# Kernel optimization log

Measured on AMD Instinct MI355X. Metric: run time of the kernel, lower is better.

The kernel has to match this reference:

```python
import jax, jax.numpy as jnp
import numpy as np

B, T, HID = 4, 2048, 1024
H, DK, DV, K = 8, 64, 128, 4
EPS = 1e-5


def _dw_causal_conv(x, w, b):
    # x: (B,T,C), w: (C,1,K) depthwise, b: (C,). Causal: left-pad K-1.
    xt = jnp.transpose(x, (0, 2, 1))  # (B,C,T)
    y = jax.lax.conv_general_dilated(
        xt, w, window_strides=(1,), padding=[(K - 1, 0)],
        dimension_numbers=("NCH", "OIH", "NCH"), feature_group_count=x.shape[-1])
    y = y + b[None, :, None]
    return jnp.transpose(y, (0, 2, 1))  # (B,T,C)


def setup_inputs() -> dict:
    key = jax.random.key(0)
    ks = jax.random.split(key, 20)
    s = 0.02
    inp = {
        "x": jax.random.normal(ks[0], (B, T, HID), jnp.float32),
        "Wq": jax.random.normal(ks[1], (H * DK, HID), jnp.float32) * s,
        "Wk": jax.random.normal(ks[2], (H * DK, HID), jnp.float32) * s,
        "Wv": jax.random.normal(ks[3], (H * DV, HID), jnp.float32) * s,
        "Wa": jax.random.normal(ks[4], (H * DV, HID), jnp.float32) * s,
        "ba": jax.random.normal(ks[5], (H * DV,), jnp.float32) * s,
        "Wb": jax.random.normal(ks[6], (H, HID), jnp.float32) * s,
        "bb": jax.random.normal(ks[7], (H,), jnp.float32) * s,
        "Wg": jax.random.normal(ks[8], (H * DV, HID), jnp.float32) * s,
        "Wo": jax.random.normal(ks[9], (HID, H * DV), jnp.float32) * s,
        "qc_w": jax.random.normal(ks[10], (H * DK, 1, K), jnp.float32) * 0.3,
        "qc_b": jnp.zeros((H * DK,), jnp.float32),
        "kc_w": jax.random.normal(ks[11], (H * DK, 1, K), jnp.float32) * 0.3,
        "kc_b": jnp.zeros((H * DK,), jnp.float32),
        "vc_w": jax.random.normal(ks[12], (H * DV, 1, K), jnp.float32) * 0.3,
        "vc_b": jnp.zeros((H * DV,), jnp.float32),
        "ln_w": jnp.ones((DV,), jnp.float32),
        "ln_b": jnp.zeros((DV,), jnp.float32),
    }
    return inp


def _forward(x, Wq, Wk, Wv, Wa, ba, Wb, bb, Wg, Wo,
             qc_w, qc_b, kc_w, kc_b, vc_w, vc_b, ln_w, ln_b):
    b, t = x.shape[0], x.shape[1]
    scale = DK ** -0.5
    q = x @ Wq.T
    k = x @ Wk.T
    v = x @ Wv.T
    q = jax.nn.silu(_dw_causal_conv(q, qc_w, qc_b))
    k = jax.nn.silu(_dw_causal_conv(k, kc_w, kc_b))
    v = jax.nn.silu(_dw_causal_conv(v, vc_w, vc_b))
    q = q.reshape(b, t, H, DK)
    k = (k * scale).reshape(b, t, H, DK)
    v = v.reshape(b, t, H, DV)
    a = jax.nn.sigmoid(x @ Wa.T + ba).reshape(b, t, H, DV)
    beta = jax.nn.sigmoid(x @ Wb.T + bb)  # (B,T,H)

    # gated delta-rule recurrence over time; state S: (B,H,DK,DV)
    def step(S, ins):
        q_t, k_t, v_t, a_t, b_t = ins
        read = jnp.einsum("bhk,bhkv->bhv", k_t, S)          # (B,H,DV)
        err = read - v_t
        S = (a_t[:, :, None, :] * S
             - b_t[:, :, None, None] * k_t[..., None] * err[:, :, None, :])
        o_t = jnp.einsum("bhk,bhkv->bhv", q_t, S)
        return S, o_t

    to_tbh = lambda u: jnp.moveaxis(u, 1, 0)  # (T,B,H,...)
    S0 = jnp.zeros((b, H, DK, DV), x.dtype)
    _, o = jax.lax.scan(step, S0, (to_tbh(q), to_tbh(k), to_tbh(v),
                                   to_tbh(a), to_tbh(beta)))
    o = jnp.moveaxis(o, 0, 1)  # (B,T,H,DV)

    # LayerNorm over DV
    mu = jnp.mean(o, axis=-1, keepdims=True)
    var = jnp.mean((o - mu) ** 2, axis=-1, keepdims=True)
    o = (o - mu) * jax.lax.rsqrt(var + EPS) * ln_w + ln_b

    g = jax.nn.sigmoid(x @ Wg.T).reshape(b, t, H, DV)
    o = (o * g).reshape(b, t, H * DV)
    return o @ Wo.T


def reference(x, Wq, Wk, Wv, Wa, ba, Wb, bb, Wg, Wo,
              qc_w, qc_b, kc_w, kc_b, vc_w, vc_b, ln_w, ln_b):
    return _forward(x, Wq, Wk, Wv, Wa, ba, Wb, bb, Wg, Wo,
                    qc_w, qc_b, kc_w, kc_b, vc_w, vc_b, ln_w, ln_b)
```

## Files before the change

kernel.cpp:

```cpp
#include <hip/hip_runtime.h>
#include <hip/hip_bf16.h>
#include <cstdint>
#include <cstddef>

#define TDIM 2048
#define NH 8

using f32x4 = __attribute__((ext_vector_type(4))) float;
using s16x8 = __attribute__((ext_vector_type(8))) short;

__device__ __forceinline__ float sigm(float x) { return 1.0f / (1.0f + __expf(-x)); }

#define GLDS(gp, lp)                                                          \
    __builtin_amdgcn_global_load_lds(                                         \
        (const __attribute__((address_space(1))) void*)(gp),                  \
        (__attribute__((address_space(3))) void*)(lp), 16, 0, 0)
#define GLDS4(gp, lp)                                                         \
    __builtin_amdgcn_global_load_lds(                                         \
        (const __attribute__((address_space(1))) void*)(gp),                  \
        (__attribute__((address_space(3))) void*)(lp), 4, 0, 0)

template<int CTRL>
__device__ __forceinline__ float dpp_add(float x) {
    int p = __builtin_amdgcn_mov_dpp(__float_as_int(x), CTRL, 0xF, 0xF, true);
    return x + __int_as_float(p);
}
__device__ __forceinline__ float reduce16(float x) {
    x = dpp_add<0xB1>(x);
    x = dpp_add<0x4E>(x);
    x = dpp_add<0x141>(x);
    x = dpp_add<0x140>(x);
    return x;
}

__global__ __launch_bounds__(256) void pack_f32_bf16_kernel(
    const float* __restrict__ src, __hip_bfloat16* __restrict__ dst, int n4)
{
    int i = blockIdx.x * 256 + threadIdx.x;
    if (i >= n4) return;
    float4 v = *(const float4*)(src + (size_t)i * 4);
    size_t o = (size_t)i * 4;
    dst[o + 0] = __float2bfloat16(v.x);
    dst[o + 1] = __float2bfloat16(v.y);
    dst[o + 2] = __float2bfloat16(v.z);
    dst[o + 3] = __float2bfloat16(v.w);
}

__global__ __launch_bounds__(256) void pack_w_kernel(
    const float* __restrict__ Wq, const float* __restrict__ Wk,
    const float* __restrict__ Wv, const float* __restrict__ Wa,
    const float* __restrict__ Wb, const float* __restrict__ Wg,
    __hip_bfloat16* __restrict__ dst)
{
    int e = blockIdx.x * 256 + threadIdx.x;
    int r = e >> 10, c = e & 1023;
    float vv;
    if      (r <  512) vv = Wq[(size_t)r * 1024 + c];
    else if (r < 1024) vv = Wk[(size_t)(r -  512) * 1024 + c];
    else if (r < 2048) vv = Wv[(size_t)(r - 1024) * 1024 + c];
    else if (r < 3072) vv = Wa[(size_t)(r - 2048) * 1024 + c];
    else if (r < 3080) vv = Wb[(size_t)(r - 3072) * 1024 + c];
    else if (r < 4104) vv = Wg[(size_t)(r - 3080) * 1024 + c];
    else               vv = 0.0f;
    dst[e] = __float2bfloat16(vv);
}

#define G1STAGE(BUF, K0) do {                                                 \
    GLDS(Ag + (K0), &At[BUF][srow * 32 + skk]);                               \
    GLDS(Ag + (K0) + (size_t)64 * Kd, &At[BUF][(64 + srow) * 32 + skk]);      \
    GLDS(Bg + (K0), &Bt[BUF][srow * 32 + skk]);                               \
    GLDS(Bg + (K0) + (size_t)64 * Kd, &Bt[BUF][(64 + srow) * 32 + skk]);      \
} while (0)

__global__ __launch_bounds__(256) void gemm1_kernel(
    const __hip_bfloat16* __restrict__ A, const __hip_bfloat16* __restrict__ Bw,
    float* __restrict__ qraw, float* __restrict__ kraw, float* __restrict__ vraw,
    float* __restrict__ abuf, float* __restrict__ betab, float* __restrict__ gbuf,
    const float* __restrict__ ba, const float* __restrict__ bb)
{
    constexpr int Kd = 1024;
    __shared__ __attribute__((aligned(16))) __hip_bfloat16 At[2][128 * 32];
    __shared__ __attribute__((aligned(16))) __hip_bfloat16 Bt[2][128 * 32];
    __shared__ __attribute__((aligned(16))) float Ct[4][16 * 68];
    const int tid = threadIdx.x;
    const int mBase = blockIdx.x * 128;
    const int nBase = blockIdx.y * 128;
    const int wave = tid >> 6, lane = tid & 63;
    const int wm = (wave >> 1) * 64, wn = (wave & 1) * 64;
    const int quad = lane >> 4, l16 = lane & 15;

    f32x4 acc[4][4];
    for (int i = 0; i < 4; i++)
        for (int j = 0; j < 4; j++)
            for (int r = 0; r < 4; r++) acc[i][j][r] = 0.0f;

    const int srow = tid >> 2;
    const int skk = (tid & 3) * 8;
    const __hip_bfloat16* Ag = A + (size_t)(mBase + srow) * Kd + skk;
    const __hip_bfloat16* Bg = Bw + (size_t)(nBase + srow) * Kd + skk;

    G1STAGE(0, 0);
    __syncthreads();
    for (int k0 = 0; k0 < Kd; k0 += 32) {
        const int cb = (k0 >> 5) & 1;
        if (k0 + 32 < Kd) G1STAGE(cb ^ 1, k0 + 32);
        s16x8 af[4], bfr[4];
#pragma unroll
        for (int i = 0; i < 4; i++)
            af[i] = *(const s16x8*)&At[cb][(wm + i * 16 + l16) * 32 + quad * 8];
#pragma unroll
        for (int j = 0; j < 4; j++)
            bfr[j] = *(const s16x8*)&Bt[cb][(wn + j * 16 + l16) * 32 + quad * 8];
#pragma unroll
        for (int i = 0; i < 4; i++)
#pragma unroll
            for (int j = 0; j < 4; j++)
                acc[i][j] = __builtin_amdgcn_mfma_f32_16x16x32_bf16(af[i], bfr[j], acc[i][j], 0, 0, 0);
        __syncthreads();
    }

    const int ncol = nBase + wn + l16 * 4;
    float* basep; size_t rstr; bool dosig = false; bool skip = false;
    float4 bias = make_float4(0.f, 0.f, 0.f, 0.f);
    if (ncol < 512)       { basep = qraw + ncol;          rstr = 512;  }
    else if (ncol < 1024) { basep = kraw + (ncol - 512);  rstr = 512;  }
    else if (ncol < 2048) { basep = vraw + (ncol - 1024); rstr = 1024; }
    else if (ncol < 3072) { basep = abuf + (ncol - 2048); rstr = 1024; dosig = true;
                            bias = *(const float4*)(ba + (ncol - 2048)); }
    else if (ncol < 3080) { basep = betab + (ncol - 3072); rstr = 8;   dosig = true;
                            bias = *(const float4*)(bb + (ncol - 3072)); }
    else if (ncol < 4104) { basep = gbuf + (ncol - 3080); rstr = 1024; dosig = true; }
    else                  { basep = gbuf; rstr = 0; skip = true; }

#pragma unroll
    for (int i = 0; i < 4; i++) {
#pragma unroll
        for (int j = 0; j < 4; j++)
#pragma unroll
            for (int r = 0; r < 4; r++)
                Ct[wave][(quad * 4 + r) * 68 + j * 16 + l16] = acc[i][j][r];
        __syncthreads();
#pragma unroll
        for (int p = 0; p < 4; p++) {
            int rr = p * 4 + quad;
            float4 val = *(const float4*)&Ct[wave][rr * 68 + l16 * 4];
            if (dosig) {
                val.x = sigm(val.x + bias.x);
                val.y = sigm(val.y + bias.y);
                val.z = sigm(val.z + bias.z);
                val.w = sigm(val.w + bias.w);
            }
            int m = mBase + wm + i * 16 + rr;
            if (!skip) *(float4*)(basep + (size_t)m * rstr) = val;
        }
        __syncthreads();
    }
}

__global__ __launch_bounds__(256) void gemm2_kernel(
    const __hip_bfloat16* __restrict__ A, const __hip_bfloat16* __restrict__ Bw,
    float* __restrict__ out)
{
    constexpr int Kd = 1024;
    __shared__ __attribute__((aligned(16))) __hip_bfloat16 At[2][128 * 32];
    __shared__ __attribute__((aligned(16))) __hip_bfloat16 Bt[2][128 * 32];
    __shared__ __attribute__((aligned(16))) float Ct[4][16 * 68];
    const int tid = threadIdx.x;
    const int mBase = blockIdx.x * 128;
    const int nBase = blockIdx.y * 128;
    const int wave = tid >> 6, lane = tid & 63;
    const int wm = (wave >> 1) * 64, wn = (wave & 1) * 64;
    const int quad = lane >> 4, l16 = lane & 15;

    f32x4 acc[4][4];
    for (int i = 0; i < 4; i++)
        for (int j = 0; j < 4; j++)
            for (int r = 0; r < 4; r++) acc[i][j][r] = 0.0f;

    const int srow = tid >> 2;
    const int skk = (tid & 3) * 8;
    const __hip_bfloat16* Ag = A + (size_t)(mBase + srow) * Kd + skk;
    const __hip_bfloat16* Bg = Bw + (size_t)(nBase + srow) * Kd + skk;

    G1STAGE(0, 0);
    __syncthreads();
    for (int k0 = 0; k0 < Kd; k0 += 32) {
        const int cb = (k0 >> 5) & 1;
        if (k0 + 32 < Kd) G1STAGE(cb ^ 1, k0 + 32);
        s16x8 af[4], bfr[4];
#pragma unroll
        for (int i = 0; i < 4; i++)
            af[i] = *(const s16x8*)&At[cb][(wm + i * 16 + l16) * 32 + quad * 8];
#pragma unroll
        for (int j = 0; j < 4; j++)
            bfr[j] = *(const s16x8*)&Bt[cb][(wn + j * 16 + l16) * 32 + quad * 8];
#pragma unroll
        for (int i = 0; i < 4; i++)
#pragma unroll
            for (int j = 0; j < 4; j++)
                acc[i][j] = __builtin_amdgcn_mfma_f32_16x16x32_bf16(af[i], bfr[j], acc[i][j], 0, 0, 0);
        __syncthreads();
    }

    const int ncol = nBase + wn + l16 * 4;
    float* basep = out + ncol;
#pragma unroll
    for (int i = 0; i < 4; i++) {
#pragma unroll
        for (int j = 0; j < 4; j++)
#pragma unroll
            for (int r = 0; r < 4; r++)
                Ct[wave][(quad * 4 + r) * 68 + j * 16 + l16] = acc[i][j][r];
        __syncthreads();
#pragma unroll
        for (int p = 0; p < 4; p++) {
            int rr = p * 4 + quad;
            float4 val = *(const float4*)&Ct[wave][rr * 68 + l16 * 4];
            int m = mBase + wm + i * 16 + rr;
            *(float4*)(basep + (size_t)m * 1024) = val;
        }
        __syncthreads();
    }
}

__global__ __launch_bounds__(256) void conv_silu_fused_kernel(
    const float* __restrict__ qraw, const float* __restrict__ kraw,
    const float* __restrict__ vraw,
    const float* __restrict__ qw, const float* __restrict__ qb,
    const float* __restrict__ kw, const float* __restrict__ kb,
    const float* __restrict__ vw, const float* __restrict__ vb,
    float* __restrict__ qcb, float* __restrict__ kcb, float* __restrict__ vcb)
{
    int e = blockIdx.x * 256 + threadIdx.x;
    int c = e & 2047;
    int bt4 = e >> 11;
    int t0 = (bt4 & 511) * 4;
    int bb_ = bt4 >> 9;
    const float* src; float* dst; const float* w4; const float* bi;
    int C, cc; float scale = 1.0f;
    if (c < 512)       { src = qraw; dst = qcb; w4 = qw; bi = qb; C = 512;  cc = c; }
    else if (c < 1024) { src = kraw; dst = kcb; w4 = kw; bi = kb; C = 512;  cc = c - 512; scale = 0.125f; }
    else               { src = vraw; dst = vcb; w4 = vw; bi = vb; C = 1024; cc = c - 1024; }
    const float* wc = w4 + (size_t)cc * 4;
    const float w0 = wc[0], w1 = wc[1], w2 = wc[2], w3 = wc[3];
    const float bs = bi[cc];
    const float* s = src + ((size_t)bb_ * TDIM + t0) * C + cc;
    float x0, x1, x2;
    if (t0 == 0) { x0 = 0.f; x1 = 0.f; x2 = 0.f; }
    else { x0 = s[-3 * C]; x1 = s[-2 * C]; x2 = s[-C]; }
    const float x3 = s[0], x4 = s[C], x5 = s[2 * C], x6 = s[3 * C];
    float* d = dst + ((size_t)bb_ * TDIM + t0) * C + cc;
    float y;
    y = fmaf(w0, x0, fmaf(w1, x1, fmaf(w2, x2, fmaf(w3, x3, bs))));
    d[0] = y * sigm(y) * scale;
    y = fmaf(w0, x1, fmaf(w1, x2, fmaf(w2, x3, fmaf(w3, x4, bs))));
    d[C] = y * sigm(y) * scale;
    y = fmaf(w0, x2, fmaf(w1, x3, fmaf(w2, x4, fmaf(w3, x5, bs))));
    d[2 * C] = y * sigm(y) * scale;
    y = fmaf(w0, x3, fmaf(w1, x4, fmaf(w2, x5, fmaf(w3, x6, bs))));
    d[3 * C] = y * sigm(y) * scale;
}

#define CH 32
#define NCHUNK (TDIM / CH)

#define SCAN_STAGE_KQ(BUF, T0) do {                                           \
    _Pragma("unroll") for (int j = 0; j < 8; j++) {                           \
        int flat = j * 64 + lane;                                             \
        int tt = flat >> 4, c4 = (flat & 15) * 4;                             \
        GLDS(kc + kqB + (size_t)((T0) + tt) * 512 + c4, &kL[BUF][j * 256]);   \
        GLDS(qc + kqB + (size_t)((T0) + tt) * 512 + c4, &qL[BUF][j * 256]);   \
    }                                                                         \
} while (0)

#define LOADOPS(BUF, TT, SL) do {                                             \
    kR[SL] = *(const float4*)&kL[BUF][(TT) * 64 + ks * 4];                    \
    qR[SL] = *(const float4*)&qL[BUF][(TT) * 64 + ks * 4];                    \
    vabR[SL] = *(const float4*)&vabL[BUF][((TT) * 4 + vi) * 4];               \
} while (0)

#define CSTEP(SL, TT) do {                                                    \
    const float4 kk = kR[SL];                                                 \
    const float4 qq = qR[SL];                                                 \
    const float VV = vabR[SL].x, AA = vabR[SL].y, BB = vabR[SL].z;            \
    float as0 = AA * S0, as1 = AA * S1, as2 = AA * S2, as3 = AA * S3;         \
    float nbv = VV * (-BB);                                                   \
    float r0 = kk.x * S0, r1 = kk.y * S1;                                     \
    r0 = fmaf(kk.z, S2, r0); r1 = fmaf(kk.w, S3, r1);                         \
    float rr = reduce16(r0 + r1);                                             \
    float cc = fmaf(BB, rr, nbv);                                             \
    S0 = fmaf(-cc, kk.x, as0); float o0 = qq.x * S0;                          \
    S1 = fmaf(-cc, kk.y, as1); float o1 = qq.y * S1;                          \
    S2 = fmaf(-cc, kk.z, as2); o0 = fmaf(qq.z, S2, o0);                       \
    S3 = fmaf(-cc, kk.w, as3); o1 = fmaf(qq.w, S3, o1);                       \
    oacc[TT] = reduce16(o0 + o1);                                             \
} while (0)

__global__ __launch_bounds__(64) void scan_kernel(
    const float* __restrict__ qc, const float* __restrict__ kc,
    const float* __restrict__ vc, const float* __restrict__ ab,
    const float* __restrict__ betab, float* __restrict__ ob)
{
    __shared__ __attribute__((aligned(16))) float kL[2][CH * 64];
    __shared__ __attribute__((aligned(16))) float qL[2][CH * 64];
    __shared__ __attribute__((aligned(16))) float vabL[2][CH * 4 * 4];
    __shared__ __attribute__((aligned(16))) float oL[4 * CH];

    const int bid = blockIdx.x;
    const int bh = bid & 31, vg = bid >> 5;
    const int h = bh & 7, b = bh >> 3;
    const int lane = threadIdx.x;
    const int ks = lane & 15, vi = lane >> 4;

    const size_t kqB = (size_t)b * TDIM * 512 + (size_t)h * 64;
    const size_t vaB = (size_t)b * TDIM * 1024 + (size_t)h * 128 + (size_t)vg * 4;
    const size_t beB = (size_t)b * TDIM * 8 + h;

    const int t0p = lane >> 2, c0p = lane & 3;
    const int t1p = 16 + t0p;

    float S0 = 0, S1 = 0, S2 = 0, S3 = 0;
    float4 kR[4], qR[4], vabR[4];
    float oacc[CH];

    SCAN_STAGE_KQ(0, 0);
    {
        float v0 = vc[vaB + (size_t)t0p * 1024 + c0p];
        float a0 = ab[vaB + (size_t)t0p * 1024 + c0p];
        float e0 = betab[beB + (size_t)t0p * 8];
        float v1 = vc[vaB + (size_t)t1p * 1024 + c0p];
        float a1 = ab[vaB + (size_t)t1p * 1024 + c0p];
        float e1 = betab[beB + (size_t)t1p * 8];
        *(float4*)&vabL[0][lane * 4] = make_float4(v0, a0, e0, 0.f);
        *(float4*)&vabL[0][(64 + lane) * 4] = make_float4(v1, a1, e1, 0.f);
    }
    __syncthreads();
    LOADOPS(0, 0, 0); LOADOPS(0, 1, 1); LOADOPS(0, 2, 2); LOADOPS(0, 3, 3);

    for (int chk = 0; chk < NCHUNK; chk++) {
        const int buf = chk & 1;
        const int nb = buf ^ 1;
        const int tn = (chk + 1 < NCHUNK) ? (chk + 1) * CH : 0;
        SCAN_STAGE_KQ(nb, tn);
        const float nv0 = vc[vaB + (size_t)(tn + t0p) * 1024 + c0p];
        const float na0 = ab[vaB + (size_t)(tn + t0p) * 1024 + c0p];
        const float ne0 = betab[beB + (size_t)(tn + t0p) * 8];
        const float nv1 = vc[vaB + (size_t)(tn + t1p) * 1024 + c0p];
        const float na1 = ab[vaB + (size_t)(tn + t1p) * 1024 + c0p];
        const float ne1 = betab[beB + (size_t)(tn + t1p) * 8];
#pragma unroll
        for (int t = 0; t < CH; t++) {
            CSTEP(t & 3, t);
            if (t + 4 < CH) LOADOPS(buf, t + 4, t & 3);
        }
        *(float4*)&vabL[nb][lane * 4] = make_float4(nv0, na0, ne0, 0.f);
        *(float4*)&vabL[nb][(64 + lane) * 4] = make_float4(nv1, na1, ne1, 0.f);
        if (ks == 0) {
#pragma unroll
            for (int j = 0; j < 8; j++) {
                float4 o4 = make_float4(oacc[j * 4], oacc[j * 4 + 1],
                                        oacc[j * 4 + 2], oacc[j * 4 + 3]);
                *(float4*)&oL[vi * CH + j * 4] = o4;
            }
        }
        __syncthreads();
        if (lane < CH) {
            float4 ov = make_float4(oL[0 * CH + lane], oL[1 * CH + lane],
                                    oL[2 * CH + lane], oL[3 * CH + lane]);
            *(float4*)(ob + vaB + (size_t)(chk * CH + lane) * 1024) = ov;
        }
        LOADOPS(nb, 0, 0); LOADOPS(nb, 1, 1); LOADOPS(nb, 2, 2); LOADOPS(nb, 3, 3);
    }
}

__global__ __launch_bounds__(256) void ln_gate_kernel(
    const float* __restrict__ ob, const float* __restrict__ g,
    const float* __restrict__ lnw, const float* __restrict__ lnb,
    __hip_bfloat16* __restrict__ opr)
{
    int row = blockIdx.x * 4 + (threadIdx.x >> 6);
    int lane = threadIdx.x & 63;
    size_t base = (size_t)row * 128 + lane * 2;
    float2 xv = *(const float2*)(ob + base);
    float s = xv.x + xv.y;
#pragma unroll
    for (int m = 1; m <= 32; m <<= 1) s += __shfl_xor(s, m);
    float mean = s * (1.0f / 128.0f);
    float d0 = xv.x - mean, d1 = xv.y - mean;
    float vs = d0 * d0 + d1 * d1;
#pragma unroll
    for (int m = 1; m <= 32; m <<= 1) vs += __shfl_xor(vs, m);
    float rstd = rsqrtf(vs * (1.0f / 128.0f) + 1e-5f);
    float2 gv = *(const float2*)(g + base);
    float w0 = lnw[lane * 2], w1 = lnw[lane * 2 + 1];
    float b0 = lnb[lane * 2], b1 = lnb[lane * 2 + 1];
    opr[base] = __float2bfloat16((d0 * rstd * w0 + b0) * gv.x);
    opr[base + 1] = __float2bfloat16((d1 * rstd * w1 + b1) * gv.y);
}

extern "C" void kernel_launch(void* const* d_in, const int* in_sizes, int n_in,
                              void* d_out, int out_size, void* d_ws, size_t ws_size,
                              hipStream_t stream)
{
    const float* x    = (const float*)d_in[0];
    const float* Wq   = (const float*)d_in[1];
    const float* Wk   = (const float*)d_in[2];
    const float* Wv   = (const float*)d_in[3];
    const float* Wa   = (const float*)d_in[4];
    const float* ba   = (const float*)d_in[5];
    const float* Wb   = (const float*)d_in[6];
    const float* bb   = (const float*)d_in[7];
    const float* Wg   = (const float*)d_in[8];
    const float* Wo   = (const float*)d_in[9];
    const float* qc_w = (const float*)d_in[10];
    const float* qc_b = (const float*)d_in[11];
    const float* kc_w = (const float*)d_in[12];
    const float* kc_b = (const float*)d_in[13];
    const float* vc_w = (const float*)d_in[14];
    const float* vc_b = (const float*)d_in[15];
    const float* ln_w = (const float*)d_in[16];
    const float* ln_b = (const float*)d_in[17];
    float* out = (float*)d_out;

    char* W = (char*)d_ws;
    __hip_bfloat16* xbf  = (__hip_bfloat16*)(W + 0);
    __hip_bfloat16* wcat = (__hip_bfloat16*)(W + 16777216);
    __hip_bfloat16* wobf = (__hip_bfloat16*)(W + 25427968);
    float* qraw  = (float*)(W + 27525120);
    float* kraw  = (float*)(W + 44302336);
    float* vraw  = (float*)(W + 61079552);
    float* abuf  = (float*)(W + 94633984);
    float* betab = (float*)(W + 128188416);
    float* gbuf  = (float*)(W + 128450560);
    float* kcb   = (float*)(W + 162004992);
    float* vcb   = (float*)(W + 178782208);
    float* qcb   = (float*)xbf;
    float* obuf  = (float*)qraw;
    __hip_bfloat16* opr = (__hip_bfloat16*)vraw;

    pack_f32_bf16_kernel<<<8192, 256, 0, stream>>>(x, xbf, 2097152);
    pack_w_kernel<<<16896, 256, 0, stream>>>(Wq, Wk, Wv, Wa, Wb, Wg, wcat);
    pack_f32_bf16_kernel<<<1024, 256, 0, stream>>>(Wo, wobf, 262144);
    gemm1_kernel<<<dim3(64, 33), 256, 0, stream>>>(xbf, wcat, qraw, kraw, vraw,
                                                   abuf, betab, gbuf, ba, bb);
    conv_silu_fused_kernel<<<16384, 256, 0, stream>>>(
        qraw, kraw, vraw, qc_w, qc_b, kc_w, kc_b, vc_w, vc_b, qcb, kcb, vcb);
    scan_kernel<<<1024, 64, 0, stream>>>(qcb, kcb, vcb, abuf, betab, obuf);
    ln_gate_kernel<<<16384, 256, 0, stream>>>(obuf, gbuf, ln_w, ln_b, opr);
    gemm2_kernel<<<dim3(64, 8), 256, 0, stream>>>(opr, wobf, out);
}
```

Before: 500.2 us.

## Split scan state across more waves with two value columns per wave

The recurrent scan kernel now gives each 64-lane wave 2 value columns instead of 4. Each lane holds 2 key elements rather than 4, and the key reduction spans 32 lanes: a 16-lane DPP reduce followed by a v_permlane32_swap across the two half-waves. The launch doubles to 2048 blocks, and the chunk size drops to 16 timesteps so the register and LDS footprint stays small. The aim is to shorten each serial step's arithmetic and raise GPU occupancy for this latency-bound recurrence. The cost is an extra cross-half permute on every reduction and twice as many chunk barriers and global staging rounds.

```diff
diff --git a/kernel.cpp b/kernel.cpp
--- a/kernel.cpp
+++ b/kernel.cpp
@@ -15,10 +15,6 @@
     __builtin_amdgcn_global_load_lds(                                         \
         (const __attribute__((address_space(1))) void*)(gp),                  \
         (__attribute__((address_space(3))) void*)(lp), 16, 0, 0)
-#define GLDS4(gp, lp)                                                         \
-    __builtin_amdgcn_global_load_lds(                                         \
-        (const __attribute__((address_space(1))) void*)(gp),                  \
-        (__attribute__((address_space(3))) void*)(lp), 4, 0, 0)
 
 template<int CTRL>
 __device__ __forceinline__ float dpp_add(float x) {
@@ -31,6 +27,12 @@
     x = dpp_add<0x141>(x);
     x = dpp_add<0x140>(x);
     return x;
+}
+__device__ __forceinline__ float reduce32x(float x) {
+    x = reduce16(x);
+    float d = x, s = x;
+    asm("v_permlane32_swap_b32 %0, %1" : "+v"(d), "+v"(s));
+    return d + s;
 }
 
 __global__ __launch_bounds__(256) void pack_f32_bf16_kernel(
@@ -261,11 +263,11 @@
     d[3 * C] = y * sigm(y) * scale;
 }
 
-#define CH 32
+#define CH 16
 #define NCHUNK (TDIM / CH)
 
 #define SCAN_STAGE_KQ(BUF, T0) do {                                           \
-    _Pragma("unroll") for (int j = 0; j < 8; j++) {                           \
+    _Pragma("unroll") for (int j = 0; j < 4; j++) {                           \
         int flat = j * 64 + lane;                                             \
         int tt = flat >> 4, c4 = (flat & 15) * 4;                             \
         GLDS(kc + kqB + (size_t)((T0) + tt) * 512 + c4, &kL[BUF][j * 256]);   \
@@ -274,26 +276,24 @@
 } while (0)
 
 #define LOADOPS(BUF, TT, SL) do {                                             \
-    kR[SL] = *(const float4*)&kL[BUF][(TT) * 64 + ks * 4];                    \
-    qR[SL] = *(const float4*)&qL[BUF][(TT) * 64 + ks * 4];                    \
-    vabR[SL] = *(const float4*)&vabL[BUF][((TT) * 4 + vi) * 4];               \
+    kR[SL] = *(const float2*)&kL[BUF][(TT) * 64 + ks * 2];                    \
+    qR[SL] = *(const float2*)&qL[BUF][(TT) * 64 + ks * 2];                    \
+    vabR[SL] = *(const float4*)&vabL[BUF][((TT) * 2 + ci) * 4];               \
 } while (0)
 
 #define CSTEP(SL, TT) do {                                                    \
-    const float4 kk = kR[SL];                                                 \
-    const float4 qq = qR[SL];                                                 \
+    const float2 kk = kR[SL];                                                 \
+    const float2 qq = qR[SL];                                                 \
     const float VV = vabR[SL].x, AA = vabR[SL].y, BB = vabR[SL].z;            \
-    float as0 = AA * S0, as1 = AA * S1, as2 = AA * S2, as3 = AA * S3;         \
+    float as0 = AA * S0, as1 = AA * S1;                                       \
     float nbv = VV * (-BB);                                                   \
-    float r0 = kk.x * S0, r1 = kk.y * S1;                                     \
-    r0 = fmaf(kk.z, S2, r0); r1 = fmaf(kk.w, S3, r1);                         \
-    float rr = reduce16(r0 + r1);                                             \
+    float r0 = kk.x * S0;                                                     \
+    r0 = fmaf(kk.y, S1, r0);                                                  \
+    float rr = reduce32x(r0);                                                 \
     float cc = fmaf(BB, rr, nbv);                                             \
     S0 = fmaf(-cc, kk.x, as0); float o0 = qq.x * S0;                          \
-    S1 = fmaf(-cc, kk.y, as1); float o1 = qq.y * S1;                          \
-    S2 = fmaf(-cc, kk.z, as2); o0 = fmaf(qq.z, S2, o0);                       \
-    S3 = fmaf(-cc, kk.w, as3); o1 = fmaf(qq.w, S3, o1);                       \
-    oacc[TT] = reduce16(o0 + o1);                                             \
+    S1 = fmaf(-cc, kk.y, as1); o0 = fmaf(qq.y, S1, o0);                       \
+    oacc[TT] = reduce32x(o0);                                                 \
 } while (0)
 
 __global__ __launch_bounds__(64) void scan_kernel(
@@ -303,36 +303,33 @@
 {
     __shared__ __attribute__((aligned(16))) float kL[2][CH * 64];
     __shared__ __attribute__((aligned(16))) float qL[2][CH * 64];
-    __shared__ __attribute__((aligned(16))) float vabL[2][CH * 4 * 4];
-    __shared__ __attribute__((aligned(16))) float oL[4 * CH];
+    __shared__ __attribute__((aligned(16))) float vabL[2][CH * 2 * 4];
+    __shared__ __attribute__((aligned(16))) float oL[2 * CH];
 
     const int bid = blockIdx.x;
     const int bh = bid & 31, vg = bid >> 5;
     const int h = bh & 7, b = bh >> 3;
     const int lane = threadIdx.x;
-    const int ks = lane & 15, vi = lane >> 4;
+    const int ci = (lane >> 4) & 1;
+    const int ks = (lane & 15) | ((lane >> 1) & 16);
 
     const size_t kqB = (size_t)b * TDIM * 512 + (size_t)h * 64;
-    const size_t vaB = (size_t)b * TDIM * 1024 + (size_t)h * 128 + (size_t)vg * 4;
+    const size_t vaB = (size_t)b * TDIM * 1024 + (size_t)h * 128 + (size_t)vg * 2;
     const size_t beB = (size_t)b * TDIM * 8 + h;
 
-    const int t0p = lane >> 2, c0p = lane & 3;
-    const int t1p = 16 + t0p;
-
-    float S0 = 0, S1 = 0, S2 = 0, S3 = 0;
-    float4 kR[4], qR[4], vabR[4];
+    const int tvm = (lane >> 1) & 15, cv = lane & 1;
+
+    float S0 = 0, S1 = 0;
+    float2 kR[4], qR[4];
+    float4 vabR[4];
     float oacc[CH];
 
     SCAN_STAGE_KQ(0, 0);
     {
-        float v0 = vc[vaB + (size_t)t0p * 1024 + c0p];
-        float a0 = ab[vaB + (size_t)t0p * 1024 + c0p];
-        float e0 = betab[beB + (size_t)t0p * 8];
-        float v1 = vc[vaB + (size_t)t1p * 1024 + c0p];
-        float a1 = ab[vaB + (size_t)t1p * 1024 + c0p];
-        float e1 = betab[beB + (size_t)t1p * 8];
-        *(float4*)&vabL[0][lane * 4] = make_float4(v0, a0, e0, 0.f);
-        *(float4*)&vabL[0][(64 + lane) * 4] = make_float4(v1, a1, e1, 0.f);
+        float v0 = vc[vaB + (size_t)tvm * 1024 + cv];
+        float a0 = ab[vaB + (size_t)tvm * 1024 + cv];
+        float e0 = betab[beB + (size_t)tvm * 8];
+        *(float4*)&vabL[0][(tvm * 2 + cv) * 4] = make_float4(v0, a0, e0, 0.f);
     }
     __syncthreads();
     LOADOPS(0, 0, 0); LOADOPS(0, 1, 1); LOADOPS(0, 2, 2); LOADOPS(0, 3, 3);
@@ -342,32 +339,29 @@
         const int nb = buf ^ 1;
         const int tn = (chk + 1 < NCHUNK) ? (chk + 1) * CH : 0;
         SCAN_STAGE_KQ(nb, tn);
-        const float nv0 = vc[vaB + (size_t)(tn + t0p) * 1024 + c0p];
-        const float na0 = ab[vaB + (size_t)(tn + t0p) * 1024 + c0p];
-        const float ne0 = betab[beB + (size_t)(tn + t0p) * 8];
-        const float nv1 = vc[vaB + (size_t)(tn + t1p) * 1024 + c0p];
-        const float na1 = ab[vaB + (size_t)(tn + t1p) * 1024 + c0p];
-        const float ne1 = betab[beB + (size_t)(tn + t1p) * 8];
+        const float nv0 = vc[vaB + (size_t)(tn + tvm) * 1024 + cv];
+        const float na0 = ab[vaB + (size_t)(tn + tvm) * 1024 + cv];
+        const float ne0 = betab[beB + (size_t)(tn + tvm) * 8];
 #pragma unroll
         for (int t = 0; t < CH; t++) {
             CSTEP(t & 3, t);
             if (t + 4 < CH) LOADOPS(buf, t + 4, t & 3);
         }
-        *(float4*)&vabL[nb][lane * 4] = make_float4(nv0, na0, ne0, 0.f);
-        *(float4*)&vabL[nb][(64 + lane) * 4] = make_float4(nv1, na1, ne1, 0.f);
-        if (ks == 0) {
-#pragma unroll
-            for (int j = 0; j < 8; j++) {
+        *(float4*)&vabL[nb][(tvm * 2 + cv) * 4] = make_float4(nv0, na0, ne0, 0.f);
+        if ((lane & 47) == 0) {
+#pragma unroll
+            for (int j = 0; j < 4; j++) {
                 float4 o4 = make_float4(oacc[j * 4], oacc[j * 4 + 1],
                                         oacc[j * 4 + 2], oacc[j * 4 + 3]);
-                *(float4*)&oL[vi * CH + j * 4] = o4;
+                *(float4*)&oL[ci * CH + j * 4] = o4;
             }
         }
         __syncthreads();
         if (lane < CH) {
-            float4 ov = make_float4(oL[0 * CH + lane], oL[1 * CH + lane],
-                                    oL[2 * CH + lane], oL[3 * CH + lane]);
-            *(float4*)(ob + vaB + (size_t)(chk * CH + lane) * 1024) = ov;
+            float2 ov;
+            ov.x = oL[lane];
+            ov.y = oL[CH + lane];
+            *(float2*)(ob + vaB + (size_t)(chk * CH + lane) * 1024) = ov;
         }
         LOADOPS(nb, 0, 0); LOADOPS(nb, 1, 1); LOADOPS(nb, 2, 2); LOADOPS(nb, 3, 3);
     }
@@ -445,7 +439,7 @@
                                                    abuf, betab, gbuf, ba, bb);
     conv_silu_fused_kernel<<<16384, 256, 0, stream>>>(
         qraw, kraw, vraw, qc_w, qc_b, kc_w, kc_b, vc_w, vc_b, qcb, kcb, vcb);
-    scan_kernel<<<1024, 64, 0, stream>>>(qcb, kcb, vcb, abuf, betab, obuf);
+    scan_kernel<<<2048, 64, 0, stream>>>(qcb, kcb, vcb, abuf, betab, obuf);
     ln_gate_kernel<<<16384, 256, 0, stream>>>(obuf, gbuf, ln_w, ln_b, opr);
     gemm2_kernel<<<dim3(64, 8), 256, 0, stream>>>(opr, wobf, out);
 }
```

New measurement: 607.1 us. 21.4% more time.
